# Kernel tuning notes

Measured on AMD Instinct MI355X. Metric: run time of the kernel, lower is better.

## Reference

```python
import jax, jax.numpy as jnp
import numpy as np

TOPK_FRAC = 0.05
TOPK_MIN = 5
TOPK_MAX = 64


def setup_inputs() -> dict:
    key = jax.random.key(0)
    ks = jax.random.split(key, 8)
    N, H, B = 131072, 256, 512
    x = jax.random.normal(ks[0], (N, H), dtype=jnp.float32)
    batch = jnp.sort(jax.random.randint(ks[1], (N,), 0, B, dtype=jnp.int32))
    W1 = jax.random.normal(ks[2], (H, H // 2), dtype=jnp.float32) * 0.05
    b1 = jax.random.normal(ks[3], (H // 2,), dtype=jnp.float32) * 0.05
    W2 = jax.random.normal(ks[4], (H // 2, 1), dtype=jnp.float32) * 0.05
    b2 = jax.random.normal(ks[5], (1,), dtype=jnp.float32) * 0.05
    Wf = jax.random.normal(ks[6], (4 * H, H), dtype=jnp.float32) * 0.05
    bf = jax.random.normal(ks[7], (H,), dtype=jnp.float32) * 0.05
    return {"x": x, "batch": batch, "W1": W1, "b1": b1, "W2": W2,
            "b2": b2, "Wf": Wf, "bf": bf, "num_graphs": B}


def _forward(x, batch, W1, b1, W2, b2, Wf, bf, B):
    N = x.shape[0]
    # attention scores per node: MLP -> scalar
    s = (jax.nn.relu(x @ W1 + b1) @ W2 + b2)[:, 0]  # [N]
    # pyg_softmax: segment-wise stable softmax over nodes of each graph
    seg_max = jax.ops.segment_max(s, batch, num_segments=B)
    seg_max = jnp.where(jnp.isfinite(seg_max), seg_max, 0.0)  # guard empty segs
    e = jnp.exp(s - seg_max[batch])
    denom = jax.ops.segment_sum(e, batch, num_segments=B)
    w = e / denom[batch]                                    # [N]
    # pools
    x_attn = jax.ops.segment_sum(x * w[:, None], batch, num_segments=B)
    counts = jax.ops.segment_sum(jnp.ones((N,), jnp.int32), batch, num_segments=B)
    cnt_f = jnp.maximum(counts, 1).astype(x.dtype)
    x_mean = jax.ops.segment_sum(x, batch, num_segments=B) / cnt_f[:, None]
    x_max = jax.ops.segment_max(x, batch, num_segments=B)
    x_max = jnp.where(counts[:, None] > 0, x_max, 0.0)
    # per-graph dynamic k
    n = counts
    k = jnp.maximum(TOPK_MIN, jnp.ceil(TOPK_FRAC * n.astype(jnp.float32)).astype(jnp.int32))
    k = jnp.minimum(jnp.minimum(k, TOPK_MAX), n)            # [B]
    # fused segment top-k mean: sort nodes by (batch asc, w desc), keep rank<k
    order = jnp.lexsort((-w, batch))
    starts = jnp.concatenate([jnp.zeros((1,), jnp.int32), jnp.cumsum(counts)[:-1].astype(jnp.int32)])
    bs = batch[order]
    rank = jnp.arange(N, dtype=jnp.int32) - starts[bs]
    sel = (rank < k[bs]).astype(x.dtype)
    x_topk = jax.ops.segment_sum(x[order] * sel[:, None], bs, num_segments=B)
    x_topk = x_topk / jnp.maximum(k, 1).astype(x.dtype)[:, None]
    g = jax.nn.relu(jnp.concatenate([x_mean, x_attn, x_max, x_topk], axis=1) @ Wf + bf)
    return g


def reference(x, batch, W1, b1, W2, b2, Wf, bf, num_graphs):
    return _forward(x, batch, W1, b1, W2, b2, Wf, bf, num_graphs)
```

## Files before the change

kernel.cpp:

```cpp
#include <hip/hip_runtime.h>
#include <math.h>

#define N_NODES 131072
#define H 256
#define HH 128
#define B_GRAPHS 512

typedef __attribute__((ext_vector_type(8))) _Float16 half8;
typedef __attribute__((ext_vector_type(2))) _Float16 half2v;
typedef __attribute__((ext_vector_type(16))) float f32x16;

__device__ __forceinline__ uint packh(_Float16 h0, _Float16 h1) {
  half2v t;
  t[0] = h0; t[1] = h1;
  return __builtin_bit_cast(uint, t);
}

__global__ void k_prep_w1(const float* __restrict__ W1, ushort* __restrict__ W1h) {
  const int idx = blockIdx.x * 256 + threadIdx.x;
  const int k = idx >> 7, c = idx & 127;
  const float v = W1[idx];
  const _Float16 h1 = (_Float16)v;
  const float r = (v - (float)h1) * 4096.f;
  const _Float16 h2 = (_Float16)r;
  W1h[0 * 32768 + c * 256 + k] = __builtin_bit_cast(ushort, h1);
  W1h[1 * 32768 + c * 256 + k] = __builtin_bit_cast(ushort, h2);
}

__global__ void k_seg_bounds(const int* __restrict__ batch, int* __restrict__ seg_start,
                             int N, int B) {
  int b = blockIdx.x * blockDim.x + threadIdx.x;
  if (b > B) return;
  int lo = 0, hi = N;
  while (lo < hi) {
    int mid = (lo + hi) >> 1;
    if (batch[mid] < b) lo = mid + 1; else hi = mid;
  }
  seg_start[b] = lo;
}

__global__ __launch_bounds__(256, 2) void k_score_mfma(
    const float* __restrict__ x, const ushort* __restrict__ W1h,
    const float* __restrict__ b1, const float* __restrict__ W2,
    const float* __restrict__ b2, float* __restrict__ s_out) {
  __shared__ ushort smem[20480];
  const int t = threadIdx.x;
  const int lane = t & 63;
  const int w = t >> 6;
  const int wr = w >> 1, wc = w & 1;
  const int nl = lane & 31, g = lane >> 5;
  const int node0 = blockIdx.x * 128;

  const int srow = t >> 1;
  const int shalf = t & 1;

  const f32x16 zero = (f32x16)0.0f;
  f32x16 acc1[2][2], acc2[2][2];
#pragma unroll
  for (int i = 0; i < 2; ++i)
#pragma unroll
    for (int j = 0; j < 2; ++j) { acc1[i][j] = zero; acc2[i][j] = zero; }

  float4 gxA[4];
  uint4 gB[2][2];

  const float* xrow = x + (size_t)(node0 + srow) * H + shalf * 16;
  const ushort* wrow = W1h + srow * 256 + shalf * 16;

#pragma unroll
  for (int q = 0; q < 4; ++q) gxA[q] = *(const float4*)(xrow + q * 4);
#pragma unroll
  for (int p = 0; p < 2; ++p) {
    gB[p][0] = *(const uint4*)(wrow + p * 32768);
    gB[p][1] = *(const uint4*)(wrow + p * 32768 + 8);
  }

#pragma unroll
  for (int it = 0; it < 8; ++it) {
    {
      uint mainw[8], residw[8];
#pragma unroll
      for (int q = 0; q < 4; ++q) {
        const float vv[4] = {gxA[q].x, gxA[q].y, gxA[q].z, gxA[q].w};
#pragma unroll
        for (int p = 0; p < 2; ++p) {
          const float v0 = vv[2 * p], v1 = vv[2 * p + 1];
          const _Float16 h0 = (_Float16)v0, h1 = (_Float16)v1;
          const float r0 = (v0 - (float)h0) * 4096.f;
          const float r1 = (v1 - (float)h1) * 4096.f;
          mainw[2 * q + p] = packh(h0, h1);
          residw[2 * q + p] = packh((_Float16)r0, (_Float16)r1);
        }
      }
      uint4* a0 = (uint4*)&smem[0 * 5120 + srow * 40 + shalf * 16];
      uint4* a1 = (uint4*)&smem[1 * 5120 + srow * 40 + shalf * 16];
      a0[0] = make_uint4(mainw[0], mainw[1], mainw[2], mainw[3]);
      a0[1] = make_uint4(mainw[4], mainw[5], mainw[6], mainw[7]);
      a1[0] = make_uint4(residw[0], residw[1], residw[2], residw[3]);
      a1[1] = make_uint4(residw[4], residw[5], residw[6], residw[7]);
#pragma unroll
      for (int p = 0; p < 2; ++p) {
        uint4* bp = (uint4*)&smem[10240 + p * 5120 + srow * 40 + shalf * 16];
        bp[0] = gB[p][0];
        bp[1] = gB[p][1];
      }
    }
    __syncthreads();
    if (it < 7) {
      const int kc = (it + 1) * 32;
#pragma unroll
      for (int q = 0; q < 4; ++q) gxA[q] = *(const float4*)(xrow + kc + q * 4);
#pragma unroll
      for (int p = 0; p < 2; ++p) {
        gB[p][0] = *(const uint4*)(wrow + p * 32768 + kc);
        gB[p][1] = *(const uint4*)(wrow + p * 32768 + kc + 8);
      }
    }
#pragma unroll
    for (int sub = 0; sub < 2; ++sub) {
      half8 a[2][2], b[2][2];
#pragma unroll
      for (int p = 0; p < 2; ++p) {
#pragma unroll
        for (int i = 0; i < 2; ++i)
          a[p][i] = *(const half8*)&smem[p * 5120 + (wr * 64 + i * 32 + nl) * 40 +
                                         sub * 16 + g * 8];
#pragma unroll
        for (int j = 0; j < 2; ++j)
          b[p][j] = *(const half8*)&smem[10240 + p * 5120 + (wc * 64 + j * 32 + nl) * 40 +
                                         sub * 16 + g * 8];
      }
#pragma unroll
      for (int i = 0; i < 2; ++i)
#pragma unroll
        for (int j = 0; j < 2; ++j) {
          acc1[i][j] = __builtin_amdgcn_mfma_f32_32x32x16_f16(a[0][i], b[0][j], acc1[i][j], 0, 0, 0);
          acc2[i][j] = __builtin_amdgcn_mfma_f32_32x32x16_f16(a[0][i], b[1][j], acc2[i][j], 0, 0, 0);
          acc2[i][j] = __builtin_amdgcn_mfma_f32_32x32x16_f16(a[1][i], b[0][j], acc2[i][j], 0, 0, 0);
        }
    }
    __syncthreads();
  }

  float* part = (float*)smem;
  const float inv4096 = 2.44140625e-4f;
  const int col0 = wc * 64 + nl;
  const float b1v0 = b1[col0], b1v1 = b1[col0 + 32];
  const float w2v0 = W2[col0], w2v1 = W2[col0 + 32];
#pragma unroll
  for (int i = 0; i < 2; ++i) {
#pragma unroll
    for (int r = 0; r < 16; ++r) {
      const int nodeL = wr * 64 + i * 32 + (r & 3) + 8 * (r >> 2) + 4 * g;
      const float h0 = acc1[i][0][r] + acc2[i][0][r] * inv4096 + b1v0;
      const float h1 = acc1[i][1][r] + acc2[i][1][r] * inv4096 + b1v1;
      const float p = fmaxf(h0, 0.f) * w2v0 + fmaxf(h1, 0.f) * w2v1;
      part[nodeL * 64 + wc * 32 + nl] = p;
    }
  }
  __syncthreads();
  if (t < 128) {
    float sv = b2[0];
#pragma unroll 8
    for (int cc = 0; cc < 64; ++cc) {
      const int c2 = (cc + t) & 63;
      sv += part[t * 64 + c2];
    }
    s_out[node0 + t] = sv;
  }
}

__global__ __launch_bounds__(512) void k_pool_fused(const float* __restrict__ x,
                                                    const float* __restrict__ s,
                                                    const int* __restrict__ seg_start,
                                                    float* __restrict__ pooled) {
  const int b = blockIdx.x;
  const int t = threadIdx.x;
  const int start = seg_start[b];
  const int end = seg_start[b + 1];
  const int n = end - start;

  __shared__ float s_lds[1024];
  __shared__ float red[512];
  __shared__ float thr_sh;
  __shared__ int thri_sh;
  __shared__ float r4[8][264];

  const bool fits = (n <= 1024);
  if (fits) {
    for (int i = t; i < n; i += 512) s_lds[i] = s[start + i];
  }
  __syncthreads();
  const float* sseg = fits ? s_lds : (s + start);

  float m = -INFINITY;
  for (int i = t; i < n; i += 512) m = fmaxf(m, sseg[i]);
  red[t] = m;
  __syncthreads();
  for (int off = 256; off > 0; off >>= 1) {
    if (t < off) red[t] = fmaxf(red[t], red[t + off]);
    __syncthreads();
  }
  const float smax = red[0];
  __syncthreads();
  float d = 0.f;
  for (int i = t; i < n; i += 512) d += __expf(sseg[i] - smax);
  red[t] = d;
  __syncthreads();
  for (int off = 256; off > 0; off >>= 1) {
    if (t < off) red[t] += red[t + off];
    __syncthreads();
  }
  const float denom = red[0];
  __syncthreads();
  const float inv_denom = (denom > 0.f) ? 1.f / denom : 0.f;

  int k = 0;
  if (n > 0) {
    k = (int)ceilf(0.05f * (float)n);
    if (k < 5) k = 5;
    if (k > 64) k = 64;
    if (k > n) k = n;
  }

  if (t < 64) {
    float pk = INFINITY;
    int pidx = -1;
    for (int r = 0; r < k; ++r) {
      float bk = -INFINITY;
      int bi = 0x7fffffff;
      for (int i = t; i < n; i += 64) {
        const float si = sseg[i];
        const int gi = start + i;
        const bool below = (si < pk) || (si == pk && gi > pidx);
        if (below && (si > bk || (si == bk && gi < bi))) { bk = si; bi = gi; }
      }
#pragma unroll
      for (int off = 32; off > 0; off >>= 1) {
        const float ok = __shfl_xor(bk, off);
        const int oi = __shfl_xor(bi, off);
        if (ok > bk || (ok == bk && oi < bi)) { bk = ok; bi = oi; }
      }
      pk = bk;
      pidx = bi;
    }
    if (t == 0) {
      thr_sh = (k > 0) ? pk : INFINITY;
      thri_sh = (k > 0) ? pidx : -1;
    }
  }
  __syncthreads();
  const float thr = thr_sh;
  const int thri = thri_sh;

  const int fq = t & 63;
  const int sub = t >> 6;
  float mean[4] = {0.f, 0.f, 0.f, 0.f};
  float attn[4] = {0.f, 0.f, 0.f, 0.f};
  float tk[4] = {0.f, 0.f, 0.f, 0.f};
  float mx[4] = {-INFINITY, -INFINITY, -INFINITY, -INFINITY};
  for (int i = sub; i < n; i += 8) {
    const float si = sseg[i];
    const float wi = __expf(si - smax);
    const int gi = start + i;
    const bool sel = (si > thr) || (si == thr && gi <= thri);
    const float4 xv = *reinterpret_cast<const float4*>(x + (size_t)gi * H + fq * 4);
    mean[0] += xv.x; mean[1] += xv.y; mean[2] += xv.z; mean[3] += xv.w;
    attn[0] = fmaf(xv.x, wi, attn[0]);
    attn[1] = fmaf(xv.y, wi, attn[1]);
    attn[2] = fmaf(xv.z, wi, attn[2]);
    attn[3] = fmaf(xv.w, wi, attn[3]);
    mx[0] = fmaxf(mx[0], xv.x);
    mx[1] = fmaxf(mx[1], xv.y);
    mx[2] = fmaxf(mx[2], xv.z);
    mx[3] = fmaxf(mx[3], xv.w);
    if (sel) {
      tk[0] += xv.x; tk[1] += xv.y; tk[2] += xv.z; tk[3] += xv.w;
    }
  }
  float* po = pooled + (size_t)b * 1024;
  const float invn = 1.f / (float)(n > 0 ? n : 1);
  const float invk = (k > 0) ? 1.f / (float)k : 0.f;
  *reinterpret_cast<float4*>(&r4[sub][fq * 4]) = make_float4(mean[0], mean[1], mean[2], mean[3]);
  __syncthreads();
  if (t < 256) {
    float tot = 0.f;
#pragma unroll
    for (int q = 0; q < 8; ++q) tot += r4[q][t];
    po[t] = tot * invn;
  }
  __syncthreads();
  *reinterpret_cast<float4*>(&r4[sub][fq * 4]) = make_float4(attn[0], attn[1], attn[2], attn[3]);
  __syncthreads();
  if (t < 256) {
    float tot = 0.f;
#pragma unroll
    for (int q = 0; q < 8; ++q) tot += r4[q][t];
    po[256 + t] = tot * inv_denom;
  }
  __syncthreads();
  *reinterpret_cast<float4*>(&r4[sub][fq * 4]) = make_float4(mx[0], mx[1], mx[2], mx[3]);
  __syncthreads();
  if (t < 256) {
    float tot = -INFINITY;
#pragma unroll
    for (int q = 0; q < 8; ++q) tot = fmaxf(tot, r4[q][t]);
    po[512 + t] = (n > 0) ? tot : 0.f;
  }
  __syncthreads();
  *reinterpret_cast<float4*>(&r4[sub][fq * 4]) = make_float4(tk[0], tk[1], tk[2], tk[3]);
  __syncthreads();
  if (t < 256) {
    float tot = 0.f;
#pragma unroll
    for (int q = 0; q < 8; ++q) tot += r4[q][t];
    po[768 + t] = tot * invk;
  }
}

__global__ __launch_bounds__(256) void k_gemm(const float* __restrict__ pooled,
                                              const float* __restrict__ Wf,
                                              float* __restrict__ gacc) {
  const int t = threadIdx.x;
  const int r0 = blockIdx.x * 8;
  const int kc0 = blockIdx.y * 128;
  __shared__ float ps[8][132];
  {
    const int r = t >> 5;
    const int c = (t & 31) << 2;
    *reinterpret_cast<float4*>(&ps[r][c]) =
        *reinterpret_cast<const float4*>(pooled + (size_t)(r0 + r) * 1024 + kc0 + c);
  }
  __syncthreads();
  float acc[8];
#pragma unroll
  for (int r = 0; r < 8; ++r) acc[r] = 0.f;
#pragma unroll 4
  for (int c = 0; c < 128; ++c) {
    const float wf = Wf[(size_t)(kc0 + c) * 256 + t];
#pragma unroll
    for (int r = 0; r < 8; ++r) acc[r] = fmaf(ps[r][c], wf, acc[r]);
  }
  float* go = gacc + ((size_t)blockIdx.y * B_GRAPHS + r0) * 256;
#pragma unroll
  for (int r = 0; r < 8; ++r) go[r * 256 + t] = acc[r];
}

__global__ __launch_bounds__(256) void k_out(const float* __restrict__ gacc,
                                             const float* __restrict__ bf,
                                             float* __restrict__ out) {
  const int i = blockIdx.x * 256 + threadIdx.x;
  float v = bf[i & 255];
#pragma unroll
  for (int ks = 0; ks < 8; ++ks) v += gacc[(size_t)ks * (B_GRAPHS * 256) + i];
  out[i] = fmaxf(v, 0.f);
}

extern "C" void kernel_launch(void* const* d_in, const int* in_sizes, int n_in,
                              void* d_out, int out_size, void* d_ws, size_t ws_size,
                              hipStream_t stream) {
  const float* x  = (const float*)d_in[0];
  const int* batch = (const int*)d_in[1];
  const float* W1 = (const float*)d_in[2];
  const float* b1 = (const float*)d_in[3];
  const float* W2 = (const float*)d_in[4];
  const float* b2 = (const float*)d_in[5];
  const float* Wf = (const float*)d_in[6];
  const float* bf = (const float*)d_in[7];
  const int N = in_sizes[1];
  const int B = B_GRAPHS;

  float* ws = (float*)d_ws;
  float* s = ws;
  int* seg_start = (int*)(ws + N);
  float* pooled = ws + N + 1024;
  float* gacc = pooled + (size_t)B * 1024;
  ushort* W1h = (ushort*)(gacc + (size_t)8 * B * 256);

  k_prep_w1<<<dim3(128), dim3(256), 0, stream>>>(W1, W1h);
  k_seg_bounds<<<dim3((B + 1 + 255) / 256), dim3(256), 0, stream>>>(batch, seg_start, N, B);
  k_score_mfma<<<dim3(N / 128), dim3(256), 0, stream>>>(x, W1h, b1, W2, b2, s);
  k_pool_fused<<<dim3(B), dim3(512), 0, stream>>>(x, s, seg_start, pooled);
  k_gemm<<<dim3(B / 8, 8), dim3(256), 0, stream>>>(pooled, Wf, gacc);
  k_out<<<dim3((B * 256) / 256), dim3(256), 0, stream>>>(gacc, bf, (float*)d_out);
}
```

Baseline: 124.7 us.

## Widen score GEMM K-tile to 64 and pre-swizzle W1 into MFMA fragment layout

The split-fp16 score GEMM now stages 64-wide K chunks instead of 32, halving the main loop to 4 iterations and so halving the block barriers. W1 is pre-packed into an MFMA-fragment-ordered layout, so B-tile global loads are contiguous and LDS fragment reads come straight from 8-element groups. The A tile uses a 76-element padded row stride to avoid bank conflicts. The cost is more shared memory per block (about 70 KB) and more registers for prefetch, which may lower occupancy.

```diff
diff --git a/kernel.cpp b/kernel.cpp
--- a/kernel.cpp
+++ b/kernel.cpp
@@ -1,30 +1,23 @@
 #include <hip/hip_runtime.h>
 #include <math.h>
 
-#define N_NODES 131072
 #define H 256
 #define HH 128
 #define B_GRAPHS 512
 
 typedef __attribute__((ext_vector_type(8))) _Float16 half8;
-typedef __attribute__((ext_vector_type(2))) _Float16 half2v;
 typedef __attribute__((ext_vector_type(16))) float f32x16;
 
-__device__ __forceinline__ uint packh(_Float16 h0, _Float16 h1) {
-  half2v t;
-  t[0] = h0; t[1] = h1;
-  return __builtin_bit_cast(uint, t);
-}
-
-__global__ void k_prep_w1(const float* __restrict__ W1, ushort* __restrict__ W1h) {
+__global__ void k_prep_w1(const float* __restrict__ W1, ushort* __restrict__ W1f) {
   const int idx = blockIdx.x * 256 + threadIdx.x;
   const int k = idx >> 7, c = idx & 127;
   const float v = W1[idx];
   const _Float16 h1 = (_Float16)v;
   const float r = (v - (float)h1) * 4096.f;
   const _Float16 h2 = (_Float16)r;
-  W1h[0 * 32768 + c * 256 + k] = __builtin_bit_cast(ushort, h1);
-  W1h[1 * 32768 + c * 256 + k] = __builtin_bit_cast(ushort, h2);
+  const int base = (((k >> 4) * 2 + ((k >> 3) & 1)) * 128 + c) * 8 + (k & 7);
+  W1f[base] = __builtin_bit_cast(ushort, h1);
+  W1f[32768 + base] = __builtin_bit_cast(ushort, h2);
 }
 
 __global__ void k_seg_bounds(const int* __restrict__ batch, int* __restrict__ seg_start,
@@ -39,11 +32,23 @@
   seg_start[b] = lo;
 }
 
+__device__ __forceinline__ void split8(const float4 v0, const float4 v1, half8& m, half8& r) {
+  const float vals[8] = {v0.x, v0.y, v0.z, v0.w, v1.x, v1.y, v1.z, v1.w};
+#pragma unroll
+  for (int e = 0; e < 8; ++e) {
+    const _Float16 h = (_Float16)vals[e];
+    m[e] = h;
+    r[e] = (_Float16)((vals[e] - (float)h) * 4096.f);
+  }
+}
+
 __global__ __launch_bounds__(256, 2) void k_score_mfma(
-    const float* __restrict__ x, const ushort* __restrict__ W1h,
+    const float* __restrict__ x, const ushort* __restrict__ W1f,
     const float* __restrict__ b1, const float* __restrict__ W2,
     const float* __restrict__ b2, float* __restrict__ s_out) {
-  __shared__ ushort smem[20480];
+  __shared__ ushort smem[35840];
+  ushort* ash = smem;
+  ushort* bsh = smem + 19456;
   const int t = threadIdx.x;
   const int lane = t & 63;
   const int w = t >> 6;
@@ -51,9 +56,6 @@
   const int nl = lane & 31, g = lane >> 5;
   const int node0 = blockIdx.x * 128;
 
-  const int srow = t >> 1;
-  const int shalf = t & 1;
-
   const f32x16 zero = (f32x16)0.0f;
   f32x16 acc1[2][2], acc2[2][2];
 #pragma unroll
@@ -61,82 +63,70 @@
 #pragma unroll
     for (int j = 0; j < 2; ++j) { acc1[i][j] = zero; acc2[i][j] = zero; }
 
-  float4 gxA[4];
-  uint4 gB[2][2];
-
-  const float* xrow = x + (size_t)(node0 + srow) * H + shalf * 16;
-  const ushort* wrow = W1h + srow * 256 + shalf * 16;
-
-#pragma unroll
-  for (int q = 0; q < 4; ++q) gxA[q] = *(const float4*)(xrow + q * 4);
-#pragma unroll
-  for (int p = 0; p < 2; ++p) {
-    gB[p][0] = *(const uint4*)(wrow + p * 32768);
-    gB[p][1] = *(const uint4*)(wrow + p * 32768 + 8);
-  }
-
-#pragma unroll
-  for (int it = 0; it < 8; ++it) {
-    {
-      uint mainw[8], residw[8];
+  const int arow = t >> 3;
+  const int acol = (t & 7) * 8;
+  const float* agsrc = x + (size_t)(node0 + arow) * H + acol;
+  const int bp = t >> 7;
+  const int boff = (t & 127) * 64;
+  const ushort* bgsrc = W1f + bp * 32768 + boff;
+
+  float4 gxa[4][2];
+  uint4 gxb[8];
+#pragma unroll
+  for (int q = 0; q < 4; ++q) {
+    gxa[q][0] = *(const float4*)(agsrc + q * 32 * H);
+    gxa[q][1] = *(const float4*)(agsrc + q * 32 * H + 4);
+  }
+#pragma unroll
+  for (int j = 0; j < 8; ++j) gxb[j] = *(const uint4*)(bgsrc + j * 8);
+
+#pragma unroll
+  for (int it = 0; it < 4; ++it) {
+#pragma unroll
+    for (int q = 0; q < 4; ++q) {
+      half8 m8, r8;
+      split8(gxa[q][0], gxa[q][1], m8, r8);
+      const int R = q * 32 + arow;
+      *(uint4*)&ash[0 * 9728 + R * 76 + acol] = __builtin_bit_cast(uint4, m8);
+      *(uint4*)&ash[1 * 9728 + R * 76 + acol] = __builtin_bit_cast(uint4, r8);
+    }
+#pragma unroll
+    for (int j = 0; j < 8; ++j)
+      *(uint4*)&bsh[bp * 8192 + boff + j * 8] = gxb[j];
+    __syncthreads();
+    if (it < 3) {
+      const int kc = (it + 1) * 64;
 #pragma unroll
       for (int q = 0; q < 4; ++q) {
-        const float vv[4] = {gxA[q].x, gxA[q].y, gxA[q].z, gxA[q].w};
-#pragma unroll
-        for (int p = 0; p < 2; ++p) {
-          const float v0 = vv[2 * p], v1 = vv[2 * p + 1];
-          const _Float16 h0 = (_Float16)v0, h1 = (_Float16)v1;
-          const float r0 = (v0 - (float)h0) * 4096.f;
-          const float r1 = (v1 - (float)h1) * 4096.f;
-          mainw[2 * q + p] = packh(h0, h1);
-          residw[2 * q + p] = packh((_Float16)r0, (_Float16)r1);
-        }
-      }
-      uint4* a0 = (uint4*)&smem[0 * 5120 + srow * 40 + shalf * 16];
-      uint4* a1 = (uint4*)&smem[1 * 5120 + srow * 40 + shalf * 16];
-      a0[0] = make_uint4(mainw[0], mainw[1], mainw[2], mainw[3]);
-      a0[1] = make_uint4(mainw[4], mainw[5], mainw[6], mainw[7]);
-      a1[0] = make_uint4(residw[0], residw[1], residw[2], residw[3]);
-      a1[1] = make_uint4(residw[4], residw[5], residw[6], residw[7]);
-#pragma unroll
-      for (int p = 0; p < 2; ++p) {
-        uint4* bp = (uint4*)&smem[10240 + p * 5120 + srow * 40 + shalf * 16];
-        bp[0] = gB[p][0];
-        bp[1] = gB[p][1];
-      }
-    }
-    __syncthreads();
-    if (it < 7) {
-      const int kc = (it + 1) * 32;
-#pragma unroll
-      for (int q = 0; q < 4; ++q) gxA[q] = *(const float4*)(xrow + kc + q * 4);
-#pragma unroll
-      for (int p = 0; p < 2; ++p) {
-        gB[p][0] = *(const uint4*)(wrow + p * 32768 + kc);
-        gB[p][1] = *(const uint4*)(wrow + p * 32768 + kc + 8);
-      }
-    }
-#pragma unroll
-    for (int sub = 0; sub < 2; ++sub) {
-      half8 a[2][2], b[2][2];
-#pragma unroll
-      for (int p = 0; p < 2; ++p) {
-#pragma unroll
-        for (int i = 0; i < 2; ++i)
-          a[p][i] = *(const half8*)&smem[p * 5120 + (wr * 64 + i * 32 + nl) * 40 +
-                                         sub * 16 + g * 8];
-#pragma unroll
-        for (int j = 0; j < 2; ++j)
-          b[p][j] = *(const half8*)&smem[10240 + p * 5120 + (wc * 64 + j * 32 + nl) * 40 +
-                                         sub * 16 + g * 8];
+        gxa[q][0] = *(const float4*)(agsrc + q * 32 * H + kc);
+        gxa[q][1] = *(const float4*)(agsrc + q * 32 * H + kc + 4);
+      }
+#pragma unroll
+      for (int j = 0; j < 8; ++j)
+        gxb[j] = *(const uint4*)(bgsrc + (it + 1) * 8192 + j * 8);
+    }
+#pragma unroll
+    for (int sub = 0; sub < 4; ++sub) {
+      half8 a0[2], a1[2], b0[2], b1[2];
+#pragma unroll
+      for (int i = 0; i < 2; ++i) {
+        const int R = wr * 64 + i * 32 + nl;
+        a0[i] = *(const half8*)&ash[0 * 9728 + R * 76 + sub * 16 + g * 8];
+        a1[i] = *(const half8*)&ash[1 * 9728 + R * 76 + sub * 16 + g * 8];
+      }
+#pragma unroll
+      for (int j = 0; j < 2; ++j) {
+        const int col = wc * 64 + j * 32 + nl;
+        b0[j] = *(const half8*)&bsh[0 * 8192 + ((sub * 2 + g) * 128 + col) * 8];
+        b1[j] = *(const half8*)&bsh[1 * 8192 + ((sub * 2 + g) * 128 + col) * 8];
       }
 #pragma unroll
       for (int i = 0; i < 2; ++i)
 #pragma unroll
         for (int j = 0; j < 2; ++j) {
-          acc1[i][j] = __builtin_amdgcn_mfma_f32_32x32x16_f16(a[0][i], b[0][j], acc1[i][j], 0, 0, 0);
-          acc2[i][j] = __builtin_amdgcn_mfma_f32_32x32x16_f16(a[0][i], b[1][j], acc2[i][j], 0, 0, 0);
-          acc2[i][j] = __builtin_amdgcn_mfma_f32_32x32x16_f16(a[1][i], b[0][j], acc2[i][j], 0, 0, 0);
+          acc1[i][j] = __builtin_amdgcn_mfma_f32_32x32x16_f16(a0[i], b0[j], acc1[i][j], 0, 0, 0);
+          acc2[i][j] = __builtin_amdgcn_mfma_f32_32x32x16_f16(a0[i], b1[j], acc2[i][j], 0, 0, 0);
+          acc2[i][j] = __builtin_amdgcn_mfma_f32_32x32x16_f16(a1[i], b0[j], acc2[i][j], 0, 0, 0);
         }
     }
     __syncthreads();
@@ -163,8 +153,7 @@
     float sv = b2[0];
 #pragma unroll 8
     for (int cc = 0; cc < 64; ++cc) {
-      const int c2 = (cc + t) & 63;
-      sv += part[t * 64 + c2];
+      sv += part[t * 64 + ((cc + t) & 63)];
     }
     s_out[node0 + t] = sv;
   }
@@ -375,11 +364,11 @@
   int* seg_start = (int*)(ws + N);
   float* pooled = ws + N + 1024;
   float* gacc = pooled + (size_t)B * 1024;
-  ushort* W1h = (ushort*)(gacc + (size_t)8 * B * 256);
-
-  k_prep_w1<<<dim3(128), dim3(256), 0, stream>>>(W1, W1h);
+  ushort* W1f = (ushort*)(gacc + (size_t)8 * B * 256);
+
+  k_prep_w1<<<dim3(128), dim3(256), 0, stream>>>(W1, W1f);
   k_seg_bounds<<<dim3((B + 1 + 255) / 256), dim3(256), 0, stream>>>(batch, seg_start, N, B);
-  k_score_mfma<<<dim3(N / 128), dim3(256), 0, stream>>>(x, W1h, b1, W2, b2, s);
+  k_score_mfma<<<dim3(N / 128), dim3(256), 0, stream>>>(x, W1f, b1, W2, b2, s);
   k_pool_fused<<<dim3(B), dim3(512), 0, stream>>>(x, s, seg_start, pooled);
   k_gemm<<<dim3(B / 8, 8), dim3(256), 0, stream>>>(pooled, Wf, gacc);
   k_out<<<dim3((B * 256) / 256), dim3(256), 0, stream>>>(gacc, bf, (float*)d_out);
```

Measured after the change: 146.9 us. 17.8% more time.
